# Kernel optimization log

Measured on AMD Instinct MI355X. Metric: run time of the kernel, lower is better.

## Reference

```python
import jax, jax.numpy as jnp
import numpy as np

# Model dims (match init_kwargs)
B, N, COORD, F0 = 16, 512, 3, 64
K = 8            # kernels per layer
F1, F2 = 128, 256  # conv filters
POOL = 2
FC = 512
EPS = 1e-9


def _pairwise(C):
    """Pairwise euclidean distances D [B,N,N] and direction cosines Cos [B,N,N] from coords C [B,N,3]."""
    dot = jnp.einsum('bic,bjc->bij', C, C)
    l2 = jnp.einsum('bic,bic->bi', C, C)
    d2 = l2[:, :, None] + l2[:, None, :] - 2.0 * dot
    D = jnp.sqrt(jnp.abs(d2) + EPS)
    nrm = jnp.sqrt(l2 + EPS)
    Cos = dot / (nrm[:, :, None] * nrm[:, None, :])
    return D, Cos


def _layer(V, D, Cos, gkw, gkb, acw, acb, gcw, gcb, bng, bnb):
    """GraphKernels -> AngularContribution -> GraphConv -> tanh -> batchnorm (eval)."""
    b, n, f = V.shape
    # GraphKernels: node-dependent learned Gaussian decay over pairwise distances
    u = jax.nn.softplus(V @ gkw + gkb)                # [B,N,K]
    uk = jnp.transpose(u, (0, 2, 1))[..., None]       # [B,K,N,1]
    A = jnp.exp(-(D[:, None] ** 2) * uk)              # [B,K,N,N]
    # AngularContribution: learned interpolation between isotropic and cosine-weighted kernel
    w = jax.nn.sigmoid(V @ acw + acb)                 # [B,N,K]
    wk = jnp.transpose(w, (0, 2, 1))[..., None]       # [B,K,N,1]
    A = A * (wk * Cos[:, None] + (1.0 - wk))          # [B,K,N,N]
    # GraphConv: per-kernel message passing then shared dense over [self || messages]
    M = jnp.einsum('bkij,bjf->bikf', A, V).reshape(b, n, -1)  # [B,N,K*F]
    H = jnp.concatenate([V, M], axis=-1) @ gcw + gcb           # [B,N,F_out]
    H = jnp.tanh(H)
    # batchnorm in eval mode (moving mean 0, var 1): affine only
    return bng * H + bnb


def _pool(V, C, p):
    """AverageSeqGraphPool: average consecutive (sequence-ordered) nodes with window/stride p."""
    b, n, f = V.shape
    return V.reshape(b, n // p, p, f).mean(2), C.reshape(b, n // p, p, -1).mean(2)


def setup_inputs() -> dict:
    key = jax.random.key(0)
    ks = jax.random.split(key, 12)
    def w(k, shape):
        return jax.random.normal(k, shape, jnp.float32) / np.sqrt(shape[0])
    flat_dim = (N // POOL // POOL) * F2
    return {
        'V': jax.random.normal(ks[0], (B, N, F0), jnp.float32),
        'C': jax.random.normal(ks[1], (B, N, COORD), jnp.float32) * 10.0,  # ~Angstrom-scale coords
        'gk_w0': w(ks[2], (F0, K)), 'gk_b0': jnp.zeros((K,), jnp.float32),
        'ac_w0': w(ks[3], (F0, K)), 'ac_b0': jnp.zeros((K,), jnp.float32),
        'gc_w0': w(ks[4], ((K + 1) * F0, F1)), 'gc_b0': jnp.zeros((F1,), jnp.float32),
        'bn_g0': jnp.ones((F1,), jnp.float32), 'bn_b0': jnp.zeros((F1,), jnp.float32),
        'gk_w1': w(ks[5], (F1, K)), 'gk_b1': jnp.zeros((K,), jnp.float32),
        'ac_w1': w(ks[6], (F1, K)), 'ac_b1': jnp.zeros((K,), jnp.float32),
        'gc_w1': w(ks[7], ((K + 1) * F1, F2)), 'gc_b1': jnp.zeros((F2,), jnp.float32),
        'bn_g1': jnp.ones((F2,), jnp.float32), 'bn_b1': jnp.zeros((F2,), jnp.float32),
        'fc_w': w(ks[8], (flat_dim, FC)), 'fc_b': jnp.zeros((FC,), jnp.float32),
    }


def reference(V, C, gk_w0, gk_b0, ac_w0, ac_b0, gc_w0, gc_b0, bn_g0, bn_b0,
              gk_w1, gk_b1, ac_w1, ac_b1, gc_w1, gc_b1, bn_g1, bn_b1, fc_w, fc_b):
    D, Cos = _pairwise(C)
    H = _layer(V, D, Cos, gk_w0, gk_b0, ac_w0, ac_b0, gc_w0, gc_b0, bn_g0, bn_b0)
    H, C1 = _pool(H, C, POOL)
    D, Cos = _pairwise(C1)
    H = _layer(H, D, Cos, gk_w1, gk_b1, ac_w1, ac_b1, gc_w1, gc_b1, bn_g1, bn_b1)
    H, _ = _pool(H, C1, POOL)
    Flat = H.reshape(H.shape[0], -1)  # [B, 128*256]
    return jax.nn.sigmoid(Flat @ fc_w + fc_b)  # [B, 512]
```

## Files before the change

kernel.cpp:

```cpp
#include <hip/hip_runtime.h>
#include <math.h>

#define KK 8
#define EPSF 1e-9f

typedef unsigned int   uint32;
typedef unsigned short u16;
typedef __attribute__((ext_vector_type(8))) short bf16x8;
typedef __attribute__((ext_vector_type(4))) float f32x4;

#define MFMA_16x16x32(a, b, c) __builtin_amdgcn_mfma_f32_16x16x32_bf16(a, b, c, 0, 0, 0)

typedef __attribute__((address_space(1))) const unsigned int glob_cu32;
typedef __attribute__((address_space(3))) unsigned int lds_u32;
__device__ __forceinline__ void g2l16(const void* gsrc, void* ldst) {
    __builtin_amdgcn_global_load_lds((glob_cu32*)gsrc, (lds_u32*)ldst, 16, 0, 0);
}

__device__ __forceinline__ int swz(int row, int o) {
    return (row << 6) + (((o) ^ (row & 7)) << 3);
}

__device__ __forceinline__ float softplusf(float x) {
    return x > 0.0f ? x + log1pf(expf(-x)) : log1pf(expf(x));
}
__device__ __forceinline__ float sigmoidf_(float x) {
    return 1.0f / (1.0f + expf(-x));
}
__device__ __forceinline__ u16 f2bf(float f) {
    union { float f; uint32 u; } v; v.f = f;
    uint32 u = v.u;
    return (u16)((u + 0x7FFFu + ((u >> 16) & 1u)) >> 16);
}
__device__ __forceinline__ uint32 pack2(float a, float b) {
    return (uint32)f2bf(a) | ((uint32)f2bf(b) << 16);
}

__global__ __launch_bounds__(256)
void prep_kernel(const float* __restrict__ V, const float* __restrict__ W0,
                 const float* __restrict__ W1, u16* __restrict__ VT0,
                 u16* __restrict__ Wt0, u16* __restrict__ Wt1) {
    __shared__ float s[64][65];
    int blk = blockIdx.x, tid = threadIdx.x;
    if (blk < 128) {
        int b = blk >> 3, rt = blk & 7;
#pragma unroll
        for (int t = 0; t < 16; t++) {
            int idx = t * 256 + tid; int r = idx >> 6, c = idx & 63;
            s[r][c] = V[((size_t)b * 512 + rt * 64 + r) * 64 + c];
        }
        __syncthreads();
#pragma unroll
        for (int t = 0; t < 16; t++) {
            int idx = t * 256 + tid; int f = idx >> 6, j = idx & 63;
            VT0[((size_t)b * 64 + f) * 512 + rt * 64 + j] = f2bf(s[j][f]);
        }
    } else if (blk < 146) {
        int t0 = blk - 128; int rt = t0 >> 1, ct = t0 & 1;
#pragma unroll
        for (int t = 0; t < 16; t++) {
            int idx = t * 256 + tid; int r = idx >> 6, c = idx & 63;
            s[r][c] = W0[((size_t)rt * 64 + r) * 128 + ct * 64 + c];
        }
        __syncthreads();
#pragma unroll
        for (int t = 0; t < 16; t++) {
            int idx = t * 256 + tid; int f = idx >> 6, j = idx & 63;
            Wt0[((size_t)ct * 64 + f) * 576 + rt * 64 + j] = f2bf(s[j][f]);
        }
    } else {
        int t0 = blk - 146; int rt = t0 >> 2, ct = t0 & 3;
#pragma unroll
        for (int t = 0; t < 16; t++) {
            int idx = t * 256 + tid; int r = idx >> 6, c = idx & 63;
            s[r][c] = W1[((size_t)rt * 64 + r) * 256 + ct * 64 + c];
        }
        __syncthreads();
#pragma unroll
        for (int t = 0; t < 16; t++) {
            int idx = t * 256 + tid; int f = idx >> 6, j = idx & 63;
            Wt1[((size_t)ct * 64 + f) * 1152 + rt * 64 + j] = f2bf(s[j][f]);
        }
    }
}

__global__ __launch_bounds__(256)
void layer0_fused(const u16* __restrict__ VT0, const float* __restrict__ C,
                  const float* __restrict__ V,
                  const float* __restrict__ gw, const float* __restrict__ gb,
                  const float* __restrict__ aw, const float* __restrict__ ab,
                  const u16* __restrict__ Wt0, const float* __restrict__ bias,
                  const float* __restrict__ bng, const float* __restrict__ bnb,
                  float* __restrict__ H0p, u16* __restrict__ VT1) {
    int b = blockIdx.x >> 5, tile = blockIdx.x & 31;
    int i0 = tile * 16;
    int tid = threadIdx.x;
    int wv = tid >> 6, lane = tid & 63, quad = lane >> 4, l15 = lane & 15;

    __shared__ __align__(16) u16 s_mem[12288];
    __shared__ __align__(16) u16 s_X[16 * 584];
    __shared__ __align__(16) float s_ci[16][4];
    __shared__ float s_u[16][KK];
    __shared__ float s_w[16][KK];

    u16* s_vT = s_mem;
    u16* s_A  = s_mem + 4096;

    {
        int t = tid & 127;
        int i = t >> 3, k = t & 7;
        const float4* xr = (const float4*)(V + ((size_t)b * 512 + i0 + i) * 64);
        const float* wm = (tid < 128) ? gw : aw;
        float s = 0.f;
#pragma unroll
        for (int f4 = 0; f4 < 16; f4++) {
            float4 x = xr[f4];
            s += x.x * wm[(f4 * 4 + 0) * 8 + k] + x.y * wm[(f4 * 4 + 1) * 8 + k]
               + x.z * wm[(f4 * 4 + 2) * 8 + k] + x.w * wm[(f4 * 4 + 3) * 8 + k];
        }
        if (tid < 128) s_u[i][k] = softplusf(s + gb[k]);
        else           s_w[i][k] = sigmoidf_(s + ab[k]);
    }
    if (tid < 16) {
        const float* cp = C + ((size_t)b * 512 + i0 + tid) * 3;
        float x = cp[0], y = cp[1], z = cp[2];
        s_ci[tid][0] = x; s_ci[tid][1] = y; s_ci[tid][2] = z;
        s_ci[tid][3] = x * x + y * y + z * z;
    }
    {
        int row = tid >> 4, f4 = tid & 15;
        float4 x = *(const float4*)(V + ((size_t)b * 512 + i0 + row) * 64 + f4 * 4);
        *(uint32*)&s_X[row * 584 + f4 * 4]     = pack2(x.x, x.y);
        *(uint32*)&s_X[row * 584 + f4 * 4 + 2] = pack2(x.z, x.w);
    }

    int ia = tid >> 4, jg = tid & 15;
    int oct = jg >> 1, half = (jg & 1) << 2;

    f32x4 acc[2][4] = {};
    for (int j0 = 0; j0 < 512; j0 += 64) {
        const float4* cp4 = (const float4*)(C + ((size_t)b * 512 + j0 + jg * 4) * 3);
        float4 q0 = cp4[0], q1 = cp4[1], q2 = cp4[2];
        float jx[4] = {q0.x, q0.w, q1.z, q2.y};
        float jy[4] = {q0.y, q1.x, q1.w, q2.z};
        float jz[4] = {q0.z, q1.y, q2.x, q2.w};
        __syncthreads();
#pragma unroll
        for (int p = 0; p < 2; p++) {
            int s = p * 256 + wv * 64 + lane;
            int f = s >> 3, op = s & 7;
            g2l16(VT0 + ((size_t)b * 64 + f) * 512 + j0 + ((op ^ (f & 7)) << 3),
                  (void*)(s_vT + (p * 256 + wv * 64) * 8));
        }
        {
            float cix = s_ci[ia][0], ciy = s_ci[ia][1], ciz = s_ci[ia][2], l2i = s_ci[ia][3];
            float d2a[4], csa[4];
#pragma unroll
            for (int jj = 0; jj < 4; jj++) {
                float l2j = jx[jj] * jx[jj] + jy[jj] * jy[jj] + jz[jj] * jz[jj];
                float dot = cix * jx[jj] + ciy * jy[jj] + ciz * jz[jj];
                d2a[jj] = fabsf(l2i + l2j - 2.f * dot) + EPSF;
                csa[jj] = dot / sqrtf((l2i + EPSF) * (l2j + EPSF));
            }
            const float* up = &s_u[ia][0];
            const float* wp = &s_w[ia][0];
#pragma unroll
            for (int k = 0; k < 8; k++) {
                float uu = up[k], ww = wp[k], om = 1.f - ww;
                float a0 = __expf(-d2a[0] * uu) * (ww * csa[0] + om);
                float a1 = __expf(-d2a[1] * uu) * (ww * csa[1] + om);
                float a2 = __expf(-d2a[2] * uu) * (ww * csa[2] + om);
                float a3 = __expf(-d2a[3] * uu) * (ww * csa[3] + om);
                int row = ia * 8 + k;
                uint2 pk = make_uint2(pack2(a0, a1), pack2(a2, a3));
                *(uint2*)&s_A[(row << 6) + ((oct ^ (row & 7)) << 3) + half] = pk;
            }
        }
        __syncthreads();
#pragma unroll
        for (int ks = 0; ks < 2; ks++) {
            int o = ks * 4 + quad;
            bf16x8 a0 = *(const bf16x8*)&s_A[swz(wv * 32 + l15, o)];
            bf16x8 a1 = *(const bf16x8*)&s_A[swz(wv * 32 + 16 + l15, o)];
#pragma unroll
            for (int cf = 0; cf < 4; cf++) {
                bf16x8 bv = *(const bf16x8*)&s_vT[swz(cf * 16 + l15, o)];
                acc[0][cf] = MFMA_16x16x32(a0, bv, acc[0][cf]);
                acc[1][cf] = MFMA_16x16x32(a1, bv, acc[1][cf]);
            }
        }
    }

#pragma unroll
    for (int rf = 0; rf < 2; rf++)
#pragma unroll
        for (int cf = 0; cf < 4; cf++)
#pragma unroll
            for (int r = 0; r < 4; r++) {
                int arow = wv * 32 + rf * 16 + quad * 4 + r;
                int i = arow >> 3, k = arow & 7;
                s_X[i * 584 + 64 + k * 64 + cf * 16 + l15] = f2bf(acc[rf][cf][r]);
            }
    __syncthreads();

    f32x4 acc2[2] = {};
#pragma unroll 3
    for (int kc = 0; kc < 576; kc += 64) {
#pragma unroll
        for (int ks = 0; ks < 2; ks++) {
            int o = ks * 4 + quad;
            bf16x8 av = *(const bf16x8*)&s_X[l15 * 584 + kc + o * 8];
#pragma unroll
            for (int cf = 0; cf < 2; cf++) {
                int col = wv * 32 + cf * 16 + l15;
                bf16x8 bv = *(const bf16x8*)&Wt0[(size_t)col * 576 + kc + o * 8];
                acc2[cf] = MFMA_16x16x32(av, bv, acc2[cf]);
            }
        }
    }

#pragma unroll
    for (int cf = 0; cf < 2; cf++) {
        int col = wv * 32 + cf * 16 + l15;
        float bs = bias[col], gg = bng[col], bb = bnb[col];
        float h0 = gg * tanhf(acc2[cf][0] + bs) + bb;
        float h1 = gg * tanhf(acc2[cf][1] + bs) + bb;
        float h2 = gg * tanhf(acc2[cf][2] + bs) + bb;
        float h3 = gg * tanhf(acc2[cf][3] + bs) + bb;
        float p0 = 0.5f * (h0 + h1), p1 = 0.5f * (h2 + h3);
        int pl = tile * 8 + quad * 2;
        H0p[((size_t)b * 256 + pl) * 128 + col] = p0;
        H0p[((size_t)b * 256 + pl + 1) * 128 + col] = p1;
        VT1[((size_t)b * 128 + col) * 256 + pl]     = f2bf(p0);
        VT1[((size_t)b * 128 + col) * 256 + pl + 1] = f2bf(p1);
    }
}

__global__ __launch_bounds__(256)
void layer1_fused(const u16* __restrict__ VT1, const float* __restrict__ C,
                  const float* __restrict__ H0p,
                  const float* __restrict__ gw, const float* __restrict__ gb,
                  const float* __restrict__ aw, const float* __restrict__ ab,
                  const u16* __restrict__ Wt1, const float* __restrict__ bias,
                  const float* __restrict__ bng, const float* __restrict__ bnb,
                  float* __restrict__ H1p) {
    int b = blockIdx.x >> 5, tile = blockIdx.x & 31;
    int i0 = tile * 8;
    int tid = threadIdx.x;
    int wv = tid >> 6, lane = tid & 63, quad = lane >> 4, l15 = lane & 15;

    __shared__ __align__(16) u16 s_mem[12288];
    __shared__ __align__(16) u16 s_X1[8 * 1160];
    __shared__ __align__(16) float s_ci[8][4];
    __shared__ float s_u[8][KK];
    __shared__ float s_w[8][KK];

    u16* s_vT = s_mem;
    u16* s_A  = s_mem + 8192;

    if (wv < 2) {
        int t = tid & 63;
        int i = t >> 3, k = t & 7;
        const float4* xr = (const float4*)(H0p + ((size_t)b * 256 + i0 + i) * 128);
        const float* wm = (wv == 0) ? gw : aw;
        float s = 0.f;
#pragma unroll
        for (int f4 = 0; f4 < 32; f4++) {
            float4 x = xr[f4];
            s += x.x * wm[(f4 * 4 + 0) * 8 + k] + x.y * wm[(f4 * 4 + 1) * 8 + k]
               + x.z * wm[(f4 * 4 + 2) * 8 + k] + x.w * wm[(f4 * 4 + 3) * 8 + k];
        }
        if (wv == 0) s_u[i][k] = softplusf(s + gb[k]);
        else         s_w[i][k] = sigmoidf_(s + ab[k]);
    }
    if (tid < 8) {
        const float* cp = C + ((size_t)b * 512 + 2 * (i0 + tid)) * 3;
        float x = 0.5f * (cp[0] + cp[3]);
        float y = 0.5f * (cp[1] + cp[4]);
        float z = 0.5f * (cp[2] + cp[5]);
        s_ci[tid][0] = x; s_ci[tid][1] = y; s_ci[tid][2] = z;
        s_ci[tid][3] = x * x + y * y + z * z;
    }
    {
        int row = tid >> 5, f4 = tid & 31;
        float4 x = *(const float4*)(H0p + ((size_t)b * 256 + i0 + row) * 128 + f4 * 4);
        *(uint32*)&s_X1[row * 1160 + f4 * 4]     = pack2(x.x, x.y);
        *(uint32*)&s_X1[row * 1160 + f4 * 4 + 2] = pack2(x.z, x.w);
    }

    int kh = tid >> 7, ia = (tid >> 4) & 7, jg = tid & 15;
    int oct = jg >> 1, half = (jg & 1) << 2;

    f32x4 acc[8] = {};
    for (int j0 = 0; j0 < 256; j0 += 64) {
        const float4* cp4 = (const float4*)(C + ((size_t)b * 512 + 2 * (j0 + jg * 4)) * 3);
        float4 q0 = cp4[0], q1 = cp4[1], q2 = cp4[2], q3 = cp4[3], q4 = cp4[4], q5 = cp4[5];
        float r[24] = {q0.x,q0.y,q0.z,q0.w, q1.x,q1.y,q1.z,q1.w, q2.x,q2.y,q2.z,q2.w,
                       q3.x,q3.y,q3.z,q3.w, q4.x,q4.y,q4.z,q4.w, q5.x,q5.y,q5.z,q5.w};
        float jx[4], jy[4], jz[4];
#pragma unroll
        for (int jj = 0; jj < 4; jj++) {
            jx[jj] = 0.5f * (r[6 * jj] + r[6 * jj + 3]);
            jy[jj] = 0.5f * (r[6 * jj + 1] + r[6 * jj + 4]);
            jz[jj] = 0.5f * (r[6 * jj + 2] + r[6 * jj + 5]);
        }
        __syncthreads();
#pragma unroll
        for (int p = 0; p < 4; p++) {
            int s = p * 256 + wv * 64 + lane;
            int f = s >> 3, op = s & 7;
            g2l16(VT1 + ((size_t)b * 128 + f) * 256 + j0 + ((op ^ (f & 7)) << 3),
                  (void*)(s_vT + (p * 256 + wv * 64) * 8));
        }
        {
            float cix = s_ci[ia][0], ciy = s_ci[ia][1], ciz = s_ci[ia][2], l2i = s_ci[ia][3];
            float d2a[4], csa[4];
#pragma unroll
            for (int jj = 0; jj < 4; jj++) {
                float l2j = jx[jj] * jx[jj] + jy[jj] * jy[jj] + jz[jj] * jz[jj];
                float dot = cix * jx[jj] + ciy * jy[jj] + ciz * jz[jj];
                d2a[jj] = fabsf(l2i + l2j - 2.f * dot) + EPSF;
                csa[jj] = dot / sqrtf((l2i + EPSF) * (l2j + EPSF));
            }
            const float* up = &s_u[ia][kh * 4];
            const float* wp = &s_w[ia][kh * 4];
#pragma unroll
            for (int kk = 0; kk < 4; kk++) {
                float uu = up[kk], ww = wp[kk], om = 1.f - ww;
                float a0 = __expf(-d2a[0] * uu) * (ww * csa[0] + om);
                float a1 = __expf(-d2a[1] * uu) * (ww * csa[1] + om);
                float a2 = __expf(-d2a[2] * uu) * (ww * csa[2] + om);
                float a3 = __expf(-d2a[3] * uu) * (ww * csa[3] + om);
                int row = ia * 8 + kh * 4 + kk;
                uint2 pk = make_uint2(pack2(a0, a1), pack2(a2, a3));
                *(uint2*)&s_A[(row << 6) + ((oct ^ (row & 7)) << 3) + half] = pk;
            }
        }
        __syncthreads();
#pragma unroll
        for (int ks = 0; ks < 2; ks++) {
            int o = ks * 4 + quad;
            bf16x8 a0 = *(const bf16x8*)&s_A[swz(wv * 16 + l15, o)];
#pragma unroll
            for (int cf = 0; cf < 8; cf++) {
                bf16x8 bv = *(const bf16x8*)&s_vT[swz(cf * 16 + l15, o)];
                acc[cf] = MFMA_16x16x32(a0, bv, acc[cf]);
            }
        }
    }

#pragma unroll
    for (int cf = 0; cf < 8; cf++)
#pragma unroll
        for (int r = 0; r < 4; r++) {
            int arow = wv * 16 + quad * 4 + r;
            int i = arow >> 3, k = arow & 7;
            s_X1[i * 1160 + 128 + k * 128 + cf * 16 + l15] = f2bf(acc[cf][r]);
        }
    __syncthreads();

    f32x4 acc2[4] = {};
#pragma unroll 2
    for (int kc = 0; kc < 1152; kc += 64) {
#pragma unroll
        for (int ks = 0; ks < 2; ks++) {
            int o = ks * 4 + quad;
            bf16x8 av = *(const bf16x8*)&s_X1[(l15 & 7) * 1160 + kc + o * 8];
#pragma unroll
            for (int cf = 0; cf < 4; cf++) {
                int col = wv * 64 + cf * 16 + l15;
                bf16x8 bv = *(const bf16x8*)&Wt1[(size_t)col * 1152 + kc + o * 8];
                acc2[cf] = MFMA_16x16x32(av, bv, acc2[cf]);
            }
        }
    }

#pragma unroll
    for (int cf = 0; cf < 4; cf++) {
        int col = wv * 64 + cf * 16 + l15;
        float bs = bias[col], gg = bng[col], bb = bnb[col];
        float h0 = gg * tanhf(acc2[cf][0] + bs) + bb;
        float h1 = gg * tanhf(acc2[cf][1] + bs) + bb;
        float h2 = gg * tanhf(acc2[cf][2] + bs) + bb;
        float h3 = gg * tanhf(acc2[cf][3] + bs) + bb;
        if (quad < 2) {
            float p0 = 0.5f * (h0 + h1), p1 = 0.5f * (h2 + h3);
            int pl = tile * 4 + quad * 2;
            H1p[((size_t)b * 128 + pl) * 256 + col] = p0;
            H1p[((size_t)b * 128 + pl + 1) * 256 + col] = p1;
        }
    }
}

__global__ __launch_bounds__(256)
void fc_partial_kernel(const float* __restrict__ Flat, const float* __restrict__ W,
                       float* __restrict__ P) {
    int cs = blockIdx.x & 3, ks = blockIdx.x >> 2;
    int m0 = ks * 256;
    int c4 = threadIdx.x & 31;
    int msub = threadIdx.x >> 5;

    __shared__ __align__(16) float xT[256][16];

#pragma unroll
    for (int q = 0; q < 16; q++) {
        int idx = q * 256 + threadIdx.x;
        int b = idx >> 8, mm = idx & 255;
        int bg = (b >> 2) ^ (mm & 3);
        xT[mm][(bg << 2) + (b & 3)] = Flat[(size_t)b * 32768 + m0 + mm];
    }
    __syncthreads();

    const float4* W4 = (const float4*)W;
    float4 acc[16] = {};

    for (int h = 0; h < 4; h++) {
        float4 wbuf[8];
#pragma unroll
        for (int i = 0; i < 8; i++) {
            int mm = msub * 32 + h * 8 + i;
            wbuf[i] = W4[(size_t)(m0 + mm) * 128 + cs * 32 + c4];
        }
#pragma unroll
        for (int i = 0; i < 8; i++) {
            int mm = msub * 32 + h * 8 + i;
#pragma unroll
            for (int bg = 0; bg < 4; bg++) {
                float4 xv = *(const float4*)&xT[mm][((bg ^ (mm & 3)) << 2)];
                acc[bg * 4 + 0].x += xv.x * wbuf[i].x; acc[bg * 4 + 0].y += xv.x * wbuf[i].y;
                acc[bg * 4 + 0].z += xv.x * wbuf[i].z; acc[bg * 4 + 0].w += xv.x * wbuf[i].w;
                acc[bg * 4 + 1].x += xv.y * wbuf[i].x; acc[bg * 4 + 1].y += xv.y * wbuf[i].y;
                acc[bg * 4 + 1].z += xv.y * wbuf[i].z; acc[bg * 4 + 1].w += xv.y * wbuf[i].w;
                acc[bg * 4 + 2].x += xv.z * wbuf[i].x; acc[bg * 4 + 2].y += xv.z * wbuf[i].y;
                acc[bg * 4 + 2].z += xv.z * wbuf[i].z; acc[bg * 4 + 2].w += xv.z * wbuf[i].w;
                acc[bg * 4 + 3].x += xv.w * wbuf[i].x; acc[bg * 4 + 3].y += xv.w * wbuf[i].y;
                acc[bg * 4 + 3].z += xv.w * wbuf[i].z; acc[bg * 4 + 3].w += xv.w * wbuf[i].w;
            }
        }
    }
    __syncthreads();
    __shared__ __align__(16) float red[8][32][4];
#pragma unroll
    for (int b = 0; b < 16; b++) {
        red[msub][c4][0] = acc[b].x; red[msub][c4][1] = acc[b].y;
        red[msub][c4][2] = acc[b].z; red[msub][c4][3] = acc[b].w;
        __syncthreads();
        if (msub == 0) {
            float4 s = make_float4(0.f, 0.f, 0.f, 0.f);
#pragma unroll
            for (int m = 0; m < 8; m++) {
                s.x += red[m][c4][0]; s.y += red[m][c4][1];
                s.z += red[m][c4][2]; s.w += red[m][c4][3];
            }
            *(float4*)&P[((size_t)ks * 16 + b) * 512 + cs * 128 + c4 * 4] = s;
        }
        __syncthreads();
    }
}

__global__ __launch_bounds__(256)
void fc_reduce_kernel(const float* __restrict__ P, const float* __restrict__ fcb,
                      float* __restrict__ out) {
    __shared__ float red[8][33];
    int o = blockIdx.x * 32 + (threadIdx.x & 31);
    int kg = threadIdx.x >> 5;
    float s = 0.f;
#pragma unroll
    for (int q = 0; q < 16; q++) s += P[(size_t)(kg * 16 + q) * 8192 + o];
    red[kg][threadIdx.x & 31] = s;
    __syncthreads();
    if (kg == 0) {
        float t = fcb[o & 511];
#pragma unroll
        for (int m = 0; m < 8; m++) t += red[m][threadIdx.x & 31];
        out[o] = 1.f / (1.f + expf(-t));
    }
}

extern "C" void kernel_launch(void* const* d_in, const int* in_sizes, int n_in,
                              void* d_out, int out_size, void* d_ws, size_t ws_size,
                              hipStream_t stream) {
    const float* V     = (const float*)d_in[0];
    const float* C     = (const float*)d_in[1];
    const float* gk_w0 = (const float*)d_in[2];
    const float* gk_b0 = (const float*)d_in[3];
    const float* ac_w0 = (const float*)d_in[4];
    const float* ac_b0 = (const float*)d_in[5];
    const float* gc_w0 = (const float*)d_in[6];
    const float* gc_b0 = (const float*)d_in[7];
    const float* bn_g0 = (const float*)d_in[8];
    const float* bn_b0 = (const float*)d_in[9];
    const float* gk_w1 = (const float*)d_in[10];
    const float* gk_b1 = (const float*)d_in[11];
    const float* ac_w1 = (const float*)d_in[12];
    const float* ac_b1 = (const float*)d_in[13];
    const float* gc_w1 = (const float*)d_in[14];
    const float* gc_b1 = (const float*)d_in[15];
    const float* bn_g1 = (const float*)d_in[16];
    const float* bn_b1 = (const float*)d_in[17];
    const float* fc_w  = (const float*)d_in[18];
    const float* fc_b  = (const float*)d_in[19];
    float* out = (float*)d_out;

    float* H0p = (float*)d_ws;
    float* H1p = H0p + 524288;
    float* P   = H1p + 524288;
    u16* VT0 = (u16*)(P + 1048576);
    u16* VT1 = VT0 + 524288;
    u16* Wt0 = VT1 + 524288;
    u16* Wt1 = Wt0 + 73728;

    prep_kernel<<<218, 256, 0, stream>>>(V, gc_w0, gc_w1, VT0, Wt0, Wt1);
    layer0_fused<<<512, 256, 0, stream>>>(VT0, C, V, gk_w0, gk_b0, ac_w0, ac_b0,
                                          Wt0, gc_b0, bn_g0, bn_b0, H0p, VT1);
    layer1_fused<<<512, 256, 0, stream>>>(VT1, C, H0p, gk_w1, gk_b1, ac_w1, ac_b1,
                                          Wt1, gc_b1, bn_g1, bn_b1, H1p);
    fc_partial_kernel<<<512, 256, 0, stream>>>(H1p, fc_w, P);
    fc_reduce_kernel<<<256, 256, 0, stream>>>(P, fc_b, out);
}
```

Baseline: 219.8 us.

## Double-buffer GraphConv weight tiles in LDS via async global-to-LDS loads

The dense GraphConv GEMM in both fused layer kernels previously read weight fragments directly from global memory inside the MFMA loop. It now streams 128-column by 64-k weight tiles into a swizzled, double-buffered LDS region using global_load_lds, prefetching the next tile while computing on the current one. Layer 1's 256 output columns are split into two 128-column chunks to fit the tile. This aims to hide global-load latency and coalesce the weight reads, at the cost of more LDS per block, which may lower occupancy, and an extra barrier per k-step.

```diff
diff --git a/kernel.cpp b/kernel.cpp
--- a/kernel.cpp
+++ b/kernel.cpp
@@ -97,7 +97,7 @@
     int tid = threadIdx.x;
     int wv = tid >> 6, lane = tid & 63, quad = lane >> 4, l15 = lane & 15;
 
-    __shared__ __align__(16) u16 s_mem[12288];
+    __shared__ __align__(16) u16 s_mem[16384];
     __shared__ __align__(16) u16 s_X[16 * 584];
     __shared__ __align__(16) float s_ci[16][4];
     __shared__ float s_u[16][KK];
@@ -203,17 +203,38 @@
             }
     __syncthreads();
 
+    {
+#pragma unroll
+        for (int p = 0; p < 4; p++) {
+            int s = p * 256 + wv * 64 + lane;
+            int cc = s >> 3, op = s & 7;
+            g2l16(Wt0 + (size_t)cc * 576 + ((op ^ (cc & 7)) << 3),
+                  (void*)(s_mem + (p * 256 + wv * 64) * 8));
+        }
+    }
     f32x4 acc2[2] = {};
-#pragma unroll 3
-    for (int kc = 0; kc < 576; kc += 64) {
+    for (int c = 0; c < 9; c++) {
+        u16* cur = s_mem + (c & 1) * 8192;
+        u16* nxt = s_mem + ((c + 1) & 1) * 8192;
+        __syncthreads();
+        if (c < 8) {
+            int kcn = (c + 1) * 64;
+#pragma unroll
+            for (int p = 0; p < 4; p++) {
+                int s = p * 256 + wv * 64 + lane;
+                int cc = s >> 3, op = s & 7;
+                g2l16(Wt0 + (size_t)cc * 576 + kcn + ((op ^ (cc & 7)) << 3),
+                      (void*)(nxt + (p * 256 + wv * 64) * 8));
+            }
+        }
+        int kc = c * 64;
 #pragma unroll
         for (int ks = 0; ks < 2; ks++) {
             int o = ks * 4 + quad;
             bf16x8 av = *(const bf16x8*)&s_X[l15 * 584 + kc + o * 8];
 #pragma unroll
             for (int cf = 0; cf < 2; cf++) {
-                int col = wv * 32 + cf * 16 + l15;
-                bf16x8 bv = *(const bf16x8*)&Wt0[(size_t)col * 576 + kc + o * 8];
+                bf16x8 bv = *(const bf16x8*)&cur[swz(wv * 32 + cf * 16 + l15, o)];
                 acc2[cf] = MFMA_16x16x32(av, bv, acc2[cf]);
             }
         }
@@ -249,7 +270,7 @@
     int tid = threadIdx.x;
     int wv = tid >> 6, lane = tid & 63, quad = lane >> 4, l15 = lane & 15;
 
-    __shared__ __align__(16) u16 s_mem[12288];
+    __shared__ __align__(16) u16 s_mem[16384];
     __shared__ __align__(16) u16 s_X1[8 * 1160];
     __shared__ __align__(16) float s_ci[8][4];
     __shared__ float s_u[8][KK];
@@ -359,30 +380,58 @@
         }
     __syncthreads();
 
+    {
+#pragma unroll
+        for (int p = 0; p < 4; p++) {
+            int s = p * 256 + wv * 64 + lane;
+            int cc = s >> 3, op = s & 7;
+            g2l16(Wt1 + (size_t)cc * 1152 + ((op ^ (cc & 7)) << 3),
+                  (void*)(s_mem + (p * 256 + wv * 64) * 8));
+        }
+    }
     f32x4 acc2[4] = {};
-#pragma unroll 2
-    for (int kc = 0; kc < 1152; kc += 64) {
-#pragma unroll
-        for (int ks = 0; ks < 2; ks++) {
-            int o = ks * 4 + quad;
-            bf16x8 av = *(const bf16x8*)&s_X1[(l15 & 7) * 1160 + kc + o * 8];
-#pragma unroll
-            for (int cf = 0; cf < 4; cf++) {
-                int col = wv * 64 + cf * 16 + l15;
-                bf16x8 bv = *(const bf16x8*)&Wt1[(size_t)col * 1152 + kc + o * 8];
-                acc2[cf] = MFMA_16x16x32(av, bv, acc2[cf]);
-            }
-        }
-    }
-
-#pragma unroll
-    for (int cf = 0; cf < 4; cf++) {
-        int col = wv * 64 + cf * 16 + l15;
+    int g = 0;
+    for (int ch = 0; ch < 2; ch++) {
+        for (int c = 0; c < 18; c++, g++) {
+            u16* cur = s_mem + (g & 1) * 8192;
+            u16* nxt = s_mem + ((g + 1) & 1) * 8192;
+            __syncthreads();
+            if (g < 35) {
+                int gn = g + 1;
+                int chn = (gn >= 18) ? 1 : 0;
+                int colb = chn * 128;
+                int kcn = (gn - chn * 18) * 64;
+#pragma unroll
+                for (int p = 0; p < 4; p++) {
+                    int s = p * 256 + wv * 64 + lane;
+                    int cc = s >> 3, op = s & 7;
+                    g2l16(Wt1 + (size_t)(colb + cc) * 1152 + kcn + ((op ^ (cc & 7)) << 3),
+                          (void*)(nxt + (p * 256 + wv * 64) * 8));
+                }
+            }
+            int kc = c * 64;
+#pragma unroll
+            for (int ks = 0; ks < 2; ks++) {
+                int o = ks * 4 + quad;
+                bf16x8 av = *(const bf16x8*)&s_X1[(l15 & 7) * 1160 + kc + o * 8];
+#pragma unroll
+                for (int cf = 0; cf < 2; cf++) {
+                    bf16x8 bv = *(const bf16x8*)&cur[swz(wv * 32 + cf * 16 + l15, o)];
+                    acc2[ch * 2 + cf] = MFMA_16x16x32(av, bv, acc2[ch * 2 + cf]);
+                }
+            }
+        }
+    }
+
+#pragma unroll
+    for (int q = 0; q < 4; q++) {
+        int ch = q >> 1, cf = q & 1;
+        int col = ch * 128 + wv * 32 + cf * 16 + l15;
         float bs = bias[col], gg = bng[col], bb = bnb[col];
-        float h0 = gg * tanhf(acc2[cf][0] + bs) + bb;
-        float h1 = gg * tanhf(acc2[cf][1] + bs) + bb;
-        float h2 = gg * tanhf(acc2[cf][2] + bs) + bb;
-        float h3 = gg * tanhf(acc2[cf][3] + bs) + bb;
+        float h0 = gg * tanhf(acc2[q][0] + bs) + bb;
+        float h1 = gg * tanhf(acc2[q][1] + bs) + bb;
+        float h2 = gg * tanhf(acc2[q][2] + bs) + bb;
+        float h3 = gg * tanhf(acc2[q][3] + bs) + bb;
         if (quad < 2) {
             float p0 = 0.5f * (h0 + h1), p1 = 0.5f * (h2 + h3);
             int pl = tile * 4 + quad * 2;
```

New measurement: 206.4 us. 6.1% less time.

## Double-buffer A/V tiles and stage weights through LDS with larger node tiles

Applied to the files above, without the earlier changes.

Both fused layer kernels now run 512 threads per block, and each block covers twice as many nodes, with half as many blocks. The message-passing loop is double-buffered: the next V tile is DMA'd and the next adjacency tile generated while MFMAs consume the current one, cutting one barrier per iteration. The dense GraphConv weights are streamed into LDS with async global-to-LDS copies in a double buffer instead of being read directly from global memory. This aims to overlap global loads with compute and reuse weight loads across more rows. In exchange it uses more LDS per block and launches fewer blocks, which may reduce occupancy.

```diff
diff --git a/kernel.cpp b/kernel.cpp
--- a/kernel.cpp
+++ b/kernel.cpp
@@ -84,7 +84,7 @@
     }
 }
 
-__global__ __launch_bounds__(256)
+__global__ __launch_bounds__(512)
 void layer0_fused(const u16* __restrict__ VT0, const float* __restrict__ C,
                   const float* __restrict__ V,
                   const float* __restrict__ gw, const float* __restrict__ gb,
@@ -92,25 +92,22 @@
                   const u16* __restrict__ Wt0, const float* __restrict__ bias,
                   const float* __restrict__ bng, const float* __restrict__ bnb,
                   float* __restrict__ H0p, u16* __restrict__ VT1) {
-    int b = blockIdx.x >> 5, tile = blockIdx.x & 31;
-    int i0 = tile * 16;
+    int b = blockIdx.x >> 4, tile = blockIdx.x & 15;
+    int i0 = tile * 32;
     int tid = threadIdx.x;
     int wv = tid >> 6, lane = tid & 63, quad = lane >> 4, l15 = lane & 15;
 
-    __shared__ __align__(16) u16 s_mem[12288];
-    __shared__ __align__(16) u16 s_X[16 * 584];
-    __shared__ __align__(16) float s_ci[16][4];
-    __shared__ float s_u[16][KK];
-    __shared__ float s_w[16][KK];
-
-    u16* s_vT = s_mem;
-    u16* s_A  = s_mem + 4096;
+    __shared__ __align__(16) u16 s_mem[2][20480];
+    __shared__ __align__(16) u16 s_X[32 * 584];
+    __shared__ __align__(16) float s_ci[32][4];
+    __shared__ float s_u[32][KK];
+    __shared__ float s_w[32][KK];
 
     {
-        int t = tid & 127;
+        int t = tid & 255;
         int i = t >> 3, k = t & 7;
         const float4* xr = (const float4*)(V + ((size_t)b * 512 + i0 + i) * 64);
-        const float* wm = (tid < 128) ? gw : aw;
+        const float* wm = (tid < 256) ? gw : aw;
         float s = 0.f;
 #pragma unroll
         for (int f4 = 0; f4 < 16; f4++) {
@@ -118,10 +115,10 @@
             s += x.x * wm[(f4 * 4 + 0) * 8 + k] + x.y * wm[(f4 * 4 + 1) * 8 + k]
                + x.z * wm[(f4 * 4 + 2) * 8 + k] + x.w * wm[(f4 * 4 + 3) * 8 + k];
         }
-        if (tid < 128) s_u[i][k] = softplusf(s + gb[k]);
+        if (tid < 256) s_u[i][k] = softplusf(s + gb[k]);
         else           s_w[i][k] = sigmoidf_(s + ab[k]);
     }
-    if (tid < 16) {
+    if (tid < 32) {
         const float* cp = C + ((size_t)b * 512 + i0 + tid) * 3;
         float x = cp[0], y = cp[1], z = cp[2];
         s_ci[tid][0] = x; s_ci[tid][1] = y; s_ci[tid][2] = z;
@@ -137,54 +134,70 @@
     int ia = tid >> 4, jg = tid & 15;
     int oct = jg >> 1, half = (jg & 1) << 2;
 
-    f32x4 acc[2][4] = {};
-    for (int j0 = 0; j0 < 512; j0 += 64) {
-        const float4* cp4 = (const float4*)(C + ((size_t)b * 512 + j0 + jg * 4) * 3);
-        float4 q0 = cp4[0], q1 = cp4[1], q2 = cp4[2];
+    auto dmaV = [&](int j0, u16* sV) {
+        int s = wv * 64 + lane;
+        int f = s >> 3, op = s & 7;
+        g2l16(VT0 + ((size_t)b * 64 + f) * 512 + j0 + ((op ^ (f & 7)) << 3),
+              (void*)(sV + (wv * 64) * 8));
+    };
+    auto agen = [&](float4 q0, float4 q1, float4 q2, u16* sA) {
         float jx[4] = {q0.x, q0.w, q1.z, q2.y};
         float jy[4] = {q0.y, q1.x, q1.w, q2.z};
         float jz[4] = {q0.z, q1.y, q2.x, q2.w};
-        __syncthreads();
-#pragma unroll
-        for (int p = 0; p < 2; p++) {
-            int s = p * 256 + wv * 64 + lane;
-            int f = s >> 3, op = s & 7;
-            g2l16(VT0 + ((size_t)b * 64 + f) * 512 + j0 + ((op ^ (f & 7)) << 3),
-                  (void*)(s_vT + (p * 256 + wv * 64) * 8));
-        }
-        {
-            float cix = s_ci[ia][0], ciy = s_ci[ia][1], ciz = s_ci[ia][2], l2i = s_ci[ia][3];
-            float d2a[4], csa[4];
-#pragma unroll
-            for (int jj = 0; jj < 4; jj++) {
-                float l2j = jx[jj] * jx[jj] + jy[jj] * jy[jj] + jz[jj] * jz[jj];
-                float dot = cix * jx[jj] + ciy * jy[jj] + ciz * jz[jj];
-                d2a[jj] = fabsf(l2i + l2j - 2.f * dot) + EPSF;
-                csa[jj] = dot / sqrtf((l2i + EPSF) * (l2j + EPSF));
-            }
-            const float* up = &s_u[ia][0];
-            const float* wp = &s_w[ia][0];
-#pragma unroll
-            for (int k = 0; k < 8; k++) {
-                float uu = up[k], ww = wp[k], om = 1.f - ww;
-                float a0 = __expf(-d2a[0] * uu) * (ww * csa[0] + om);
-                float a1 = __expf(-d2a[1] * uu) * (ww * csa[1] + om);
-                float a2 = __expf(-d2a[2] * uu) * (ww * csa[2] + om);
-                float a3 = __expf(-d2a[3] * uu) * (ww * csa[3] + om);
-                int row = ia * 8 + k;
-                uint2 pk = make_uint2(pack2(a0, a1), pack2(a2, a3));
-                *(uint2*)&s_A[(row << 6) + ((oct ^ (row & 7)) << 3) + half] = pk;
-            }
-        }
-        __syncthreads();
+        float cix = s_ci[ia][0], ciy = s_ci[ia][1], ciz = s_ci[ia][2], l2i = s_ci[ia][3];
+        float d2a[4], csa[4];
+#pragma unroll
+        for (int jj = 0; jj < 4; jj++) {
+            float l2j = jx[jj] * jx[jj] + jy[jj] * jy[jj] + jz[jj] * jz[jj];
+            float dot = cix * jx[jj] + ciy * jy[jj] + ciz * jz[jj];
+            d2a[jj] = fabsf(l2i + l2j - 2.f * dot) + EPSF;
+            csa[jj] = dot / sqrtf((l2i + EPSF) * (l2j + EPSF));
+        }
+        const float* up = &s_u[ia][0];
+        const float* wp = &s_w[ia][0];
+#pragma unroll
+        for (int k = 0; k < 8; k++) {
+            float uu = up[k], ww = wp[k], om = 1.f - ww;
+            float a0 = __expf(-d2a[0] * uu) * (ww * csa[0] + om);
+            float a1 = __expf(-d2a[1] * uu) * (ww * csa[1] + om);
+            float a2 = __expf(-d2a[2] * uu) * (ww * csa[2] + om);
+            float a3 = __expf(-d2a[3] * uu) * (ww * csa[3] + om);
+            int row = ia * 8 + k;
+            uint2 pk = make_uint2(pack2(a0, a1), pack2(a2, a3));
+            *(uint2*)&sA[(row << 6) + ((oct ^ (row & 7)) << 3) + half] = pk;
+        }
+    };
+
+    __syncthreads();
+
+    f32x4 acc[2][4] = {};
+    {
+        const float4* cp4 = (const float4*)(C + ((size_t)b * 512 + 0 + jg * 4) * 3);
+        float4 q0 = cp4[0], q1 = cp4[1], q2 = cp4[2];
+        agen(q0, q1, q2, s_mem[0] + 4096);
+        dmaV(0, s_mem[0]);
+    }
+    for (int n = 0; n < 8; n++) {
+        float4 q0, q1, q2;
+        if (n < 7) {
+            const float4* cp4 = (const float4*)(C + ((size_t)b * 512 + (n + 1) * 64 + jg * 4) * 3);
+            q0 = cp4[0]; q1 = cp4[1]; q2 = cp4[2];
+        }
+        __syncthreads();
+        if (n < 7) {
+            dmaV((n + 1) * 64, s_mem[(n + 1) & 1]);
+            agen(q0, q1, q2, s_mem[(n + 1) & 1] + 4096);
+        }
+        const u16* sV = s_mem[n & 1];
+        const u16* sA = s_mem[n & 1] + 4096;
 #pragma unroll
         for (int ks = 0; ks < 2; ks++) {
             int o = ks * 4 + quad;
-            bf16x8 a0 = *(const bf16x8*)&s_A[swz(wv * 32 + l15, o)];
-            bf16x8 a1 = *(const bf16x8*)&s_A[swz(wv * 32 + 16 + l15, o)];
+            bf16x8 a0 = *(const bf16x8*)&sA[swz(wv * 32 + l15, o)];
+            bf16x8 a1 = *(const bf16x8*)&sA[swz(wv * 32 + 16 + l15, o)];
 #pragma unroll
             for (int cf = 0; cf < 4; cf++) {
-                bf16x8 bv = *(const bf16x8*)&s_vT[swz(cf * 16 + l15, o)];
+                bf16x8 bv = *(const bf16x8*)&sV[swz(cf * 16 + l15, o)];
                 acc[0][cf] = MFMA_16x16x32(a0, bv, acc[0][cf]);
                 acc[1][cf] = MFMA_16x16x32(a1, bv, acc[1][cf]);
             }
@@ -203,17 +216,217 @@
             }
     __syncthreads();
 
+    u16* wbuf0 = s_mem[0];
+    u16* wbuf1 = s_mem[0] + 8192;
+    auto dmaW0 = [&](int kc, u16* buf) {
+#pragma unroll
+        for (int p = 0; p < 2; p++) {
+            int s = p * 512 + tid;
+            int cc = s >> 3, op = s & 7;
+            g2l16(Wt0 + (size_t)cc * 576 + kc + ((op ^ (cc & 7)) << 3),
+                  (void*)(buf + (p * 512 + wv * 64) * 8));
+        }
+    };
+    dmaW0(0, wbuf0);
     f32x4 acc2[2] = {};
-#pragma unroll 3
-    for (int kc = 0; kc < 576; kc += 64) {
+    int rw = wv & 1, cw = wv >> 1;
+    for (int c = 0; c < 9; c++) {
+        u16* cur = (c & 1) ? wbuf1 : wbuf0;
+        u16* nxt = (c & 1) ? wbuf0 : wbuf1;
+        __syncthreads();
+        if (c < 8) dmaW0((c + 1) * 64, nxt);
+        int kc = c * 64;
 #pragma unroll
         for (int ks = 0; ks < 2; ks++) {
             int o = ks * 4 + quad;
-            bf16x8 av = *(const bf16x8*)&s_X[l15 * 584 + kc + o * 8];
+            bf16x8 av = *(const bf16x8*)&s_X[(rw * 16 + l15) * 584 + kc + o * 8];
 #pragma unroll
             for (int cf = 0; cf < 2; cf++) {
-                int col = wv * 32 + cf * 16 + l15;
-                bf16x8 bv = *(const bf16x8*)&Wt0[(size_t)col * 576 + kc + o * 8];
+                bf16x8 bv = *(const bf16x8*)&cur[swz(cw * 32 + cf * 16 + l15, o)];
+                acc2[cf] = MFMA_16x16x32(av, bv, acc2[cf]);
+            }
+        }
+    }
+
+#pragma unroll
+    for (int cf = 0; cf < 2; cf++) {
+        int col = cw * 32 + cf * 16 + l15;
+        float bs = bias[col], gg = bng[col], bb = bnb[col];
+        float h0 = gg * tanhf(acc2[cf][0] + bs) + bb;
+        float h1 = gg * tanhf(acc2[cf][1] + bs) + bb;
+        float h2 = gg * tanhf(acc2[cf][2] + bs) + bb;
+        float h3 = gg * tanhf(acc2[cf][3] + bs) + bb;
+        float p0 = 0.5f * (h0 + h1), p1 = 0.5f * (h2 + h3);
+        int pl = tile * 16 + rw * 8 + quad * 2;
+        H0p[((size_t)b * 256 + pl) * 128 + col] = p0;
+        H0p[((size_t)b * 256 + pl + 1) * 128 + col] = p1;
+        VT1[((size_t)b * 128 + col) * 256 + pl]     = f2bf(p0);
+        VT1[((size_t)b * 128 + col) * 256 + pl + 1] = f2bf(p1);
+    }
+}
+
+__global__ __launch_bounds__(512)
+void layer1_fused(const u16* __restrict__ VT1, const float* __restrict__ C,
+                  const float* __restrict__ H0p,
+                  const float* __restrict__ gw, const float* __restrict__ gb,
+                  const float* __restrict__ aw, const float* __restrict__ ab,
+                  const u16* __restrict__ Wt1, const float* __restrict__ bias,
+                  const float* __restrict__ bng, const float* __restrict__ bnb,
+                  float* __restrict__ H1p) {
+    int b = blockIdx.x >> 4, tile = blockIdx.x & 15;
+    int i0 = tile * 16;
+    int tid = threadIdx.x;
+    int wv = tid >> 6, lane = tid & 63, quad = lane >> 4, l15 = lane & 15;
+
+    __shared__ __align__(16) u16 s_mem[2][16384];
+    __shared__ __align__(16) u16 s_X1[16 * 1160];
+    __shared__ __align__(16) float s_ci[16][4];
+    __shared__ float s_u[16][KK];
+    __shared__ float s_w[16][KK];
+
+    if (tid < 256) {
+        int t = tid & 127;
+        int i = t >> 3, k = t & 7;
+        const float4* xr = (const float4*)(H0p + ((size_t)b * 256 + i0 + i) * 128);
+        const float* wm = (tid < 128) ? gw : aw;
+        float s = 0.f;
+#pragma unroll
+        for (int f4 = 0; f4 < 32; f4++) {
+            float4 x = xr[f4];
+            s += x.x * wm[(f4 * 4 + 0) * 8 + k] + x.y * wm[(f4 * 4 + 1) * 8 + k]
+               + x.z * wm[(f4 * 4 + 2) * 8 + k] + x.w * wm[(f4 * 4 + 3) * 8 + k];
+        }
+        if (tid < 128) s_u[i][k] = softplusf(s + gb[k]);
+        else           s_w[i][k] = sigmoidf_(s + ab[k]);
+    }
+    if (tid < 16) {
+        const float* cp = C + ((size_t)b * 512 + 2 * (i0 + tid)) * 3;
+        float x = 0.5f * (cp[0] + cp[3]);
+        float y = 0.5f * (cp[1] + cp[4]);
+        float z = 0.5f * (cp[2] + cp[5]);
+        s_ci[tid][0] = x; s_ci[tid][1] = y; s_ci[tid][2] = z;
+        s_ci[tid][3] = x * x + y * y + z * z;
+    }
+    {
+        int row = tid >> 5, f4 = tid & 31;
+        float4 x = *(const float4*)(H0p + ((size_t)b * 256 + i0 + row) * 128 + f4 * 4);
+        *(uint32*)&s_X1[row * 1160 + f4 * 4]     = pack2(x.x, x.y);
+        *(uint32*)&s_X1[row * 1160 + f4 * 4 + 2] = pack2(x.z, x.w);
+    }
+
+    int kh = tid >> 8, ia = (tid >> 4) & 15, jg = tid & 15;
+    int oct = jg >> 1, half = (jg & 1) << 2;
+
+    auto dmaV = [&](int j0, u16* sV) {
+#pragma unroll
+        for (int p = 0; p < 2; p++) {
+            int s = p * 512 + tid;
+            int f = s >> 3, op = s & 7;
+            g2l16(VT1 + ((size_t)b * 128 + f) * 256 + j0 + ((op ^ (f & 7)) << 3),
+                  (void*)(sV + (p * 512 + wv * 64) * 8));
+        }
+    };
+    auto agen = [&](const float* r, u16* sA) {
+        float jx[4], jy[4], jz[4];
+#pragma unroll
+        for (int jj = 0; jj < 4; jj++) {
+            jx[jj] = 0.5f * (r[6 * jj] + r[6 * jj + 3]);
+            jy[jj] = 0.5f * (r[6 * jj + 1] + r[6 * jj + 4]);
+            jz[jj] = 0.5f * (r[6 * jj + 2] + r[6 * jj + 5]);
+        }
+        float cix = s_ci[ia][0], ciy = s_ci[ia][1], ciz = s_ci[ia][2], l2i = s_ci[ia][3];
+        float d2a[4], csa[4];
+#pragma unroll
+        for (int jj = 0; jj < 4; jj++) {
+            float l2j = jx[jj] * jx[jj] + jy[jj] * jy[jj] + jz[jj] * jz[jj];
+            float dot = cix * jx[jj] + ciy * jy[jj] + ciz * jz[jj];
+            d2a[jj] = fabsf(l2i + l2j - 2.f * dot) + EPSF;
+            csa[jj] = dot / sqrtf((l2i + EPSF) * (l2j + EPSF));
+        }
+        const float* up = &s_u[ia][kh * 4];
+        const float* wp = &s_w[ia][kh * 4];
+#pragma unroll
+        for (int kk = 0; kk < 4; kk++) {
+            float uu = up[kk], ww = wp[kk], om = 1.f - ww;
+            float a0 = __expf(-d2a[0] * uu) * (ww * csa[0] + om);
+            float a1 = __expf(-d2a[1] * uu) * (ww * csa[1] + om);
+            float a2 = __expf(-d2a[2] * uu) * (ww * csa[2] + om);
+            float a3 = __expf(-d2a[3] * uu) * (ww * csa[3] + om);
+            int row = ia * 8 + kh * 4 + kk;
+            uint2 pk = make_uint2(pack2(a0, a1), pack2(a2, a3));
+            *(uint2*)&sA[(row << 6) + ((oct ^ (row & 7)) << 3) + half] = pk;
+        }
+    };
+
+    __syncthreads();
+
+    f32x4 acc[8] = {};
+    {
+        const float4* cp4 = (const float4*)(C + ((size_t)b * 512 + 2 * (0 + jg * 4)) * 3);
+        float4 q[6]; for (int z = 0; z < 6; z++) q[z] = cp4[z];
+        agen((const float*)q, s_mem[0] + 8192);
+        dmaV(0, s_mem[0]);
+    }
+    for (int n = 0; n < 4; n++) {
+        float4 q[6];
+        if (n < 3) {
+            const float4* cp4 = (const float4*)(C + ((size_t)b * 512 + 2 * ((n + 1) * 64 + jg * 4)) * 3);
+#pragma unroll
+            for (int z = 0; z < 6; z++) q[z] = cp4[z];
+        }
+        __syncthreads();
+        if (n < 3) {
+            dmaV((n + 1) * 64, s_mem[(n + 1) & 1]);
+            agen((const float*)q, s_mem[(n + 1) & 1] + 8192);
+        }
+        const u16* sV = s_mem[n & 1];
+        const u16* sA = s_mem[n & 1] + 8192;
+#pragma unroll
+        for (int ks = 0; ks < 2; ks++) {
+            int o = ks * 4 + quad;
+            bf16x8 a0 = *(const bf16x8*)&sA[swz(wv * 16 + l15, o)];
+#pragma unroll
+            for (int cf = 0; cf < 8; cf++) {
+                bf16x8 bv = *(const bf16x8*)&sV[swz(cf * 16 + l15, o)];
+                acc[cf] = MFMA_16x16x32(a0, bv, acc[cf]);
+            }
+        }
+    }
+
+#pragma unroll
+    for (int cf = 0; cf < 8; cf++)
+#pragma unroll
+        for (int r = 0; r < 4; r++) {
+            int arow = wv * 16 + quad * 4 + r;
+            int i = arow >> 3, k = arow & 7;
+            s_X1[i * 1160 + 128 + k * 128 + cf * 16 + l15] = f2bf(acc[cf][r]);
+        }
+    __syncthreads();
+
+    auto dmaW1 = [&](int kc, u16* buf) {
+#pragma unroll
+        for (int p = 0; p < 4; p++) {
+            int s = p * 512 + tid;
+            int cc = s >> 3, op = s & 7;
+            g2l16(Wt1 + (size_t)cc * 1152 + kc + ((op ^ (cc & 7)) << 3),
+                  (void*)(buf + (p * 512 + wv * 64) * 8));
+        }
+    };
+    dmaW1(0, s_mem[0]);
+    f32x4 acc2[2] = {};
+    for (int c = 0; c < 18; c++) {
+        u16* cur = s_mem[c & 1];
+        u16* nxt = s_mem[(c + 1) & 1];
+        __syncthreads();
+        if (c < 17) dmaW1((c + 1) * 64, nxt);
+        int kc = c * 64;
+#pragma unroll
+        for (int ks = 0; ks < 2; ks++) {
+            int o = ks * 4 + quad;
+            bf16x8 av = *(const bf16x8*)&s_X1[l15 * 1160 + kc + o * 8];
+#pragma unroll
+            for (int cf = 0; cf < 2; cf++) {
+                bf16x8 bv = *(const bf16x8*)&cur[swz(wv * 32 + cf * 16 + l15, o)];
                 acc2[cf] = MFMA_16x16x32(av, bv, acc2[cf]);
             }
         }
@@ -229,166 +442,8 @@
         float h3 = gg * tanhf(acc2[cf][3] + bs) + bb;
         float p0 = 0.5f * (h0 + h1), p1 = 0.5f * (h2 + h3);
         int pl = tile * 8 + quad * 2;
-        H0p[((size_t)b * 256 + pl) * 128 + col] = p0;
-        H0p[((size_t)b * 256 + pl + 1) * 128 + col] = p1;
-        VT1[((size_t)b * 128 + col) * 256 + pl]     = f2bf(p0);
-        VT1[((size_t)b * 128 + col) * 256 + pl + 1] = f2bf(p1);
-    }
-}
-
-__global__ __launch_bounds__(256)
-void layer1_fused(const u16* __restrict__ VT1, const float* __restrict__ C,
-                  const float* __restrict__ H0p,
-                  const float* __restrict__ gw, const float* __restrict__ gb,
-                  const float* __restrict__ aw, const float* __restrict__ ab,
-                  const u16* __restrict__ Wt1, const float* __restrict__ bias,
-                  const float* __restrict__ bng, const float* __restrict__ bnb,
-                  float* __restrict__ H1p) {
-    int b = blockIdx.x >> 5, tile = blockIdx.x & 31;
-    int i0 = tile * 8;
-    int tid = threadIdx.x;
-    int wv = tid >> 6, lane = tid & 63, quad = lane >> 4, l15 = lane & 15;
-
-    __shared__ __align__(16) u16 s_mem[12288];
-    __shared__ __align__(16) u16 s_X1[8 * 1160];
-    __shared__ __align__(16) float s_ci[8][4];
-    __shared__ float s_u[8][KK];
-    __shared__ float s_w[8][KK];
-
-    u16* s_vT = s_mem;
-    u16* s_A  = s_mem + 8192;
-
-    if (wv < 2) {
-        int t = tid & 63;
-        int i = t >> 3, k = t & 7;
-        const float4* xr = (const float4*)(H0p + ((size_t)b * 256 + i0 + i) * 128);
-        const float* wm = (wv == 0) ? gw : aw;
-        float s = 0.f;
-#pragma unroll
-        for (int f4 = 0; f4 < 32; f4++) {
-            float4 x = xr[f4];
-            s += x.x * wm[(f4 * 4 + 0) * 8 + k] + x.y * wm[(f4 * 4 + 1) * 8 + k]
-               + x.z * wm[(f4 * 4 + 2) * 8 + k] + x.w * wm[(f4 * 4 + 3) * 8 + k];
-        }
-        if (wv == 0) s_u[i][k] = softplusf(s + gb[k]);
-        else         s_w[i][k] = sigmoidf_(s + ab[k]);
-    }
-    if (tid < 8) {
-        const float* cp = C + ((size_t)b * 512 + 2 * (i0 + tid)) * 3;
-        float x = 0.5f * (cp[0] + cp[3]);
-        float y = 0.5f * (cp[1] + cp[4]);
-        float z = 0.5f * (cp[2] + cp[5]);
-        s_ci[tid][0] = x; s_ci[tid][1] = y; s_ci[tid][2] = z;
-        s_ci[tid][3] = x * x + y * y + z * z;
-    }
-    {
-        int row = tid >> 5, f4 = tid & 31;
-        float4 x = *(const float4*)(H0p + ((size_t)b * 256 + i0 + row) * 128 + f4 * 4);
-        *(uint32*)&s_X1[row * 1160 + f4 * 4]     = pack2(x.x, x.y);
-        *(uint32*)&s_X1[row * 1160 + f4 * 4 + 2] = pack2(x.z, x.w);
-    }
-
-    int kh = tid >> 7, ia = (tid >> 4) & 7, jg = tid & 15;
-    int oct = jg >> 1, half = (jg & 1) << 2;
-
-    f32x4 acc[8] = {};
-    for (int j0 = 0; j0 < 256; j0 += 64) {
-        const float4* cp4 = (const float4*)(C + ((size_t)b * 512 + 2 * (j0 + jg * 4)) * 3);
-        float4 q0 = cp4[0], q1 = cp4[1], q2 = cp4[2], q3 = cp4[3], q4 = cp4[4], q5 = cp4[5];
-        float r[24] = {q0.x,q0.y,q0.z,q0.w, q1.x,q1.y,q1.z,q1.w, q2.x,q2.y,q2.z,q2.w,
-                       q3.x,q3.y,q3.z,q3.w, q4.x,q4.y,q4.z,q4.w, q5.x,q5.y,q5.z,q5.w};
-        float jx[4], jy[4], jz[4];
-#pragma unroll
-        for (int jj = 0; jj < 4; jj++) {
-            jx[jj] = 0.5f * (r[6 * jj] + r[6 * jj + 3]);
-            jy[jj] = 0.5f * (r[6 * jj + 1] + r[6 * jj + 4]);
-            jz[jj] = 0.5f * (r[6 * jj + 2] + r[6 * jj + 5]);
-        }
-        __syncthreads();
-#pragma unroll
-        for (int p = 0; p < 4; p++) {
-            int s = p * 256 + wv * 64 + lane;
-            int f = s >> 3, op = s & 7;
-            g2l16(VT1 + ((size_t)b * 128 + f) * 256 + j0 + ((op ^ (f & 7)) << 3),
-                  (void*)(s_vT + (p * 256 + wv * 64) * 8));
-        }
-        {
-            float cix = s_ci[ia][0], ciy = s_ci[ia][1], ciz = s_ci[ia][2], l2i = s_ci[ia][3];
-            float d2a[4], csa[4];
-#pragma unroll
-            for (int jj = 0; jj < 4; jj++) {
-                float l2j = jx[jj] * jx[jj] + jy[jj] * jy[jj] + jz[jj] * jz[jj];
-                float dot = cix * jx[jj] + ciy * jy[jj] + ciz * jz[jj];
-                d2a[jj] = fabsf(l2i + l2j - 2.f * dot) + EPSF;
-                csa[jj] = dot / sqrtf((l2i + EPSF) * (l2j + EPSF));
-            }
-            const float* up = &s_u[ia][kh * 4];
-            const float* wp = &s_w[ia][kh * 4];
-#pragma unroll
-            for (int kk = 0; kk < 4; kk++) {
-                float uu = up[kk], ww = wp[kk], om = 1.f - ww;
-                float a0 = __expf(-d2a[0] * uu) * (ww * csa[0] + om);
-                float a1 = __expf(-d2a[1] * uu) * (ww * csa[1] + om);
-                float a2 = __expf(-d2a[2] * uu) * (ww * csa[2] + om);
-                float a3 = __expf(-d2a[3] * uu) * (ww * csa[3] + om);
-                int row = ia * 8 + kh * 4 + kk;
-                uint2 pk = make_uint2(pack2(a0, a1), pack2(a2, a3));
-                *(uint2*)&s_A[(row << 6) + ((oct ^ (row & 7)) << 3) + half] = pk;
-            }
-        }
-        __syncthreads();
-#pragma unroll
-        for (int ks = 0; ks < 2; ks++) {
-            int o = ks * 4 + quad;
-            bf16x8 a0 = *(const bf16x8*)&s_A[swz(wv * 16 + l15, o)];
-#pragma unroll
-            for (int cf = 0; cf < 8; cf++) {
-                bf16x8 bv = *(const bf16x8*)&s_vT[swz(cf * 16 + l15, o)];
-                acc[cf] = MFMA_16x16x32(a0, bv, acc[cf]);
-            }
-        }
-    }
-
-#pragma unroll
-    for (int cf = 0; cf < 8; cf++)
-#pragma unroll
-        for (int r = 0; r < 4; r++) {
-            int arow = wv * 16 + quad * 4 + r;
-            int i = arow >> 3, k = arow & 7;
-            s_X1[i * 1160 + 128 + k * 128 + cf * 16 + l15] = f2bf(acc[cf][r]);
-        }
-    __syncthreads();
-
-    f32x4 acc2[4] = {};
-#pragma unroll 2
-    for (int kc = 0; kc < 1152; kc += 64) {
-#pragma unroll
-        for (int ks = 0; ks < 2; ks++) {
-            int o = ks * 4 + quad;
-            bf16x8 av = *(const bf16x8*)&s_X1[(l15 & 7) * 1160 + kc + o * 8];
-#pragma unroll
-            for (int cf = 0; cf < 4; cf++) {
-                int col = wv * 64 + cf * 16 + l15;
-                bf16x8 bv = *(const bf16x8*)&Wt1[(size_t)col * 1152 + kc + o * 8];
-                acc2[cf] = MFMA_16x16x32(av, bv, acc2[cf]);
-            }
-        }
-    }
-
-#pragma unroll
-    for (int cf = 0; cf < 4; cf++) {
-        int col = wv * 64 + cf * 16 + l15;
-        float bs = bias[col], gg = bng[col], bb = bnb[col];
-        float h0 = gg * tanhf(acc2[cf][0] + bs) + bb;
-        float h1 = gg * tanhf(acc2[cf][1] + bs) + bb;
-        float h2 = gg * tanhf(acc2[cf][2] + bs) + bb;
-        float h3 = gg * tanhf(acc2[cf][3] + bs) + bb;
-        if (quad < 2) {
-            float p0 = 0.5f * (h0 + h1), p1 = 0.5f * (h2 + h3);
-            int pl = tile * 4 + quad * 2;
-            H1p[((size_t)b * 128 + pl) * 256 + col] = p0;
-            H1p[((size_t)b * 128 + pl + 1) * 256 + col] = p1;
-        }
+        H1p[((size_t)b * 128 + pl) * 256 + col] = p0;
+        H1p[((size_t)b * 128 + pl + 1) * 256 + col] = p1;
     }
 }
 
@@ -511,9 +566,9 @@
     u16* Wt1 = Wt0 + 73728;
 
     prep_kernel<<<218, 256, 0, stream>>>(V, gc_w0, gc_w1, VT0, Wt0, Wt1);
-    layer0_fused<<<512, 256, 0, stream>>>(VT0, C, V, gk_w0, gk_b0, ac_w0, ac_b0,
+    layer0_fused<<<256, 512, 0, stream>>>(VT0, C, V, gk_w0, gk_b0, ac_w0, ac_b0,
                                           Wt0, gc_b0, bn_g0, bn_b0, H0p, VT1);
-    layer1_fused<<<512, 256, 0, stream>>>(VT1, C, H0p, gk_w1, gk_b1, ac_w1, ac_b1,
+    layer1_fused<<<256, 512, 0, stream>>>(VT1, C, H0p, gk_w1, gk_b1, ac_w1, ac_b1,
                                           Wt1, gc_b1, bn_g1, bn_b1, H1p);
     fc_partial_kernel<<<512, 256, 0, stream>>>(H1p, fc_w, P);
     fc_reduce_kernel<<<256, 256, 0, stream>>>(P, fc_b, out);
```

Measured after the change: 202.5 us. 7.9% less time.
